# Kernel tuning notes

Hardware: AMD Instinct MI355X
Metric: run time of the kernel (lower is better)

## Reference

```python
import jax, jax.numpy as jnp
import numpy as np

B, D, H, W = 8, 768, 32, 32
C, K = 2, 8
COORD_DIM = 128
GRID = 16
DIST_THRESH = 5
NUM_STEPS = 3
STEP_SIZE = 0.1
HW = H * W


def _pair_indices():
    # Static grid of sampled points (stride = max(1, H//grid_size)) and all
    # ordered pairs with Manhattan distance in (0, 5] -- mirrors the torch loops.
    stride = max(1, H // GRID)
    pi, pj = np.meshgrid(np.arange(0, H, stride), np.arange(0, W, stride), indexing='ij')
    pi, pj = pi.ravel(), pj.ravel()
    d = np.abs(pi[:, None] - pi[None, :]) + np.abs(pj[:, None] - pj[None, :])
    a, b = np.nonzero((d > 0) & (d <= DIST_THRESH))
    return (pi[a] * W + pj[a]).astype(np.int32), (pi[b] * W + pj[b]).astype(np.int32)


def setup_inputs() -> dict:
    key = jax.random.key(0)
    ks = jax.random.split(key, 16)
    IN = 2 * D + COORD_DIM  # 1664

    def n(i, shape, s=1.0):
        return jax.random.normal(ks[i], shape, dtype=jnp.float32) * s

    return {
        'features': n(0, (B, D, H, W)),
        'cam_raw': jax.random.uniform(ks[1], (B, C, H, W), dtype=jnp.float32),
        'y_primary': jax.random.uniform(ks[2], (B, C), dtype=jnp.float32),
        'eps': n(3, (B, K)),
        'coord_emb': n(4, (256 * 256, COORD_DIM), 0.02),
        'aff_W1': n(5, (C, IN, 256), 0.02), 'aff_b1': jnp.zeros((C, 256), jnp.float32),
        'aff_W2': n(6, (C, 256, 128), 0.05), 'aff_b2': jnp.zeros((C, 128), jnp.float32),
        'aff_W3': n(7, (C, 128, 1), 0.05), 'aff_b3': jnp.zeros((C, 1), jnp.float32),
        'mu_W1': n(8, (D, 256), 0.02), 'mu_b1': jnp.zeros((256,), jnp.float32),
        'mu_W2': n(9, (256, K), 0.05), 'mu_b2': jnp.zeros((K,), jnp.float32),
        'ls_W1': n(10, (D, 256), 0.02), 'ls_b1': jnp.zeros((256,), jnp.float32),
        'ls_W2': n(11, (256, K), 0.05), 'ls_b2': jnp.zeros((K,), jnp.float32),
        'conf_scale': jnp.array(1.0, jnp.float32),
        'conf_bias': jnp.array(0.0, jnp.float32),
    }


def reference(features, cam_raw, y_primary, eps, coord_emb,
              aff_W1, aff_b1, aff_W2, aff_b2, aff_W3, aff_b3,
              mu_W1, mu_b1, mu_W2, mu_b2, ls_W1, ls_b1, ls_W2, ls_b2,
              conf_scale, conf_bias):
    idx_a_np, idx_b_np = _pair_indices()
    idx_a, idx_b = jnp.asarray(idx_a_np), jnp.asarray(idx_b_np)
    P = idx_a.shape[0]

    # --- SubClassPosterior on globally pooled features ---
    f_global = features.mean(axis=(2, 3))                      # (B, D)
    z_mu = jax.nn.relu(f_global @ mu_W1 + mu_b1) @ mu_W2 + mu_b2
    z_logstd = jax.nn.relu(f_global @ ls_W1 + ls_b1) @ ls_W2 + ls_b2
    z_samples = z_mu + jnp.exp(z_logstd) * eps

    # --- ClassConditionalAffinity: batched gather + grouped MLP over all pairs ---
    feat = features.reshape(B, D, HW)
    f1 = feat[:, :, idx_a].transpose(0, 2, 1)                  # (B, P, D)
    f2 = feat[:, :, idx_b].transpose(0, 2, 1)                  # (B, P, D)
    ce = 0.5 * (coord_emb[idx_a] + coord_emb[idx_b])           # (P, E)
    x = jnp.concatenate([f1, f2, jnp.broadcast_to(ce, (B, P, COORD_DIM))], axis=-1)
    h = jax.nn.relu(jnp.einsum('bpi,cio->bcpo', x, aff_W1) + aff_b1[:, None, :])
    h = jax.nn.relu(jnp.einsum('bcpi,cio->bcpo', h, aff_W2) + aff_b2[:, None, :])
    logit = (jnp.einsum('bcpi,cio->bcpo', h, aff_W3) + aff_b3[:, None, :])[..., 0]
    val = jax.nn.sigmoid(logit)                                # (B, C, P)

    # A = where(mask, sigmoid(mlp), I); pairs are strictly off-diagonal & unique
    A = jnp.broadcast_to(jnp.eye(HW, dtype=features.dtype), (B, C, HW, HW))
    A = A.at[:, :, idx_a, idx_b].set(val)
    A = A / (A.sum(axis=3, keepdims=True) + 1e-8)              # row-normalize

    # --- AnisotropicDiffusion: M <- M + dt * (A M - deg * M) ---
    M = cam_raw.reshape(B, C, HW)
    deg = A.sum(axis=3)                                        # (B, C, HW)
    for _ in range(NUM_STEPS):
        L = jnp.einsum('bcij,bcj->bci', A, M) - deg * M
        M = M + STEP_SIZE * L
    cam_refined = jnp.clip(M.reshape(B, C, H, W), 0.0, 1.0)

    confidence = jax.nn.sigmoid(conf_scale * cam_refined + conf_bias)
    return cam_refined, z_mu, z_logstd, z_samples, A, confidence
```

## Files before the change

### kernel.cpp

```cpp
#include <hip/hip_runtime.h>
#include <math.h>

#define BB 8
#define DD 768
#define HWN 1024
#define NS 256
#define PPAD 3072
#define O1 256
#define O2 128

typedef __attribute__((ext_vector_type(8))) short bf16x8;
typedef __attribute__((ext_vector_type(4))) float f32x4;

__constant__ int c_du[12] = {1,-1,0,0,2,-2,0,0,1, 1,-1,-1};
__constant__ int c_dv[12] = {0, 0,1,-1,0, 0,2,-2,1,-1, 1,-1};
__constant__ signed char c_rk[25] = {
  -1,-1, 5,-1,-1,
  -1,11, 1,10,-1,
   7, 3,-1, 2, 6,
  -1, 9, 0, 8,-1,
  -1,-1, 4,-1,-1};

__device__ inline ushort f2bf(float x) {
  unsigned u = __float_as_uint(x);
  u += 0x7FFF + ((u >> 16) & 1);
  return (ushort)(u >> 16);
}
__device__ inline float bf2f(ushort h) { return __uint_as_float(((unsigned)h) << 16); }

__device__ inline bool row_sampled(int row) {
  return ((row | (row >> 5)) & 1) == 0;
}

__global__ void __launch_bounds__(256) k1(const float* __restrict__ feat,
    const float* __restrict__ cemb, const float* __restrict__ W1,
    const float* __restrict__ b1, const float* __restrict__ W2,
    float* __restrict__ fg, ushort* __restrict__ g16,
    float* __restrict__ EH, ushort* __restrict__ WT16, ushort* __restrict__ W2T16,
    float* __restrict__ A) {
  __shared__ __align__(16) float sm[64 * 65];
  int blk = blockIdx.x;
  int t = threadIdx.x;
  if (blk < 6144) {
    int row = blk;
    const float4 v = reinterpret_cast<const float4*>(feat + (size_t)row * HWN)[t];
    float s = v.x + v.y + v.z + v.w;
#pragma unroll
    for (int m = 32; m >= 1; m >>= 1) s += __shfl_xor(s, m, 64);
    if ((t & 63) == 0) sm[t >> 6] = s;
    if ((t & 8) == 0) {
      int b = row / DD, d = row - b * DD;
      int u = t >> 4, r = t & 7;
      int s1 = u * 16 + 2 * r;
      g16[((size_t)(b * NS + s1)) * DD + d] = f2bf(v.x);
      g16[((size_t)(b * NS + s1 + 1)) * DD + d] = f2bf(v.z);
    }
    __syncthreads();
    if (t == 0) fg[row] = (sm[0] + sm[1] + sm[2] + sm[3]) * (1.0f / 1024.0f);
  } else if (blk < 6656) {
    int bs = blk - 6144;
    int c = bs >> 8, s = bs & 255;
    int u = s >> 4, v = s & 15;
    int pix = (u << 6) + (v << 1);
    float* ce = sm;
    if (t < 128) ce[t] = cemb[(size_t)pix * 128 + t];
    __syncthreads();
    const float* W = W1 + ((size_t)c * 1664 + 1536) * O1;
    float acc = 0.f;
    for (int e = 0; e < 128; e++) acc = fmaf(ce[e], W[(size_t)e * O1 + t], acc);
    EH[((size_t)(c * NS + s)) * O1 + t] = 0.5f * (acc + b1[c * O1 + t]);
  } else if (blk < 6864) {
    int r0 = blk - 6656;
    const float* src; ushort* dst; int K, N, k0, n0;
    if (r0 < 192) {
      int ch = r0 / 48, r = r0 % 48;
      int c = ch & 1, half = ch >> 1;
      src = W1 + ((size_t)c * 1664 + half * 768) * 256;
      dst = WT16 + (size_t)ch * 256 * 768;
      K = 768; N = 256; k0 = (r >> 2) * 64; n0 = (r & 3) * 64;
    } else {
      int r = r0 - 192;
      int c = r >> 3; int q = r & 7;
      src = W2 + (size_t)c * 256 * 128;
      dst = W2T16 + (size_t)c * 128 * 256;
      K = 256; N = 128; k0 = (q >> 1) * 64; n0 = (q & 1) * 64;
    }
    float (*T)[65] = reinterpret_cast<float(*)[65]>(sm);
    for (int i = 0; i < 16; i++) {
      int idx = i * 256 + t; int kl = idx >> 6, nl = idx & 63;
      T[kl][nl] = src[(size_t)(k0 + kl) * N + n0 + nl];
    }
    __syncthreads();
    for (int i = 0; i < 16; i++) {
      int idx = i * 256 + t; int nl = idx >> 6, kl = idx & 63;
      dst[(size_t)(n0 + nl) * K + k0 + kl] = f2bf(T[kl][nl]);
    }
  } else {
    int r0 = (blk - 6864) * 8;
#pragma unroll
    for (int i = 0; i < 8; i++) {
      int r_g = r0 + i;
      int row = r_g & 1023;
      if (!row_sampled(row)) {
        float4 o = make_float4(0.f, 0.f, 0.f, 0.f);
        if ((row >> 2) == t) {
          float dv = 1.0f / (1.0f + 1e-8f);
          int e = row & 3;
          if (e == 0) o.x = dv; else if (e == 1) o.y = dv;
          else if (e == 2) o.z = dv; else o.w = dv;
        }
        reinterpret_cast<float4*>(A + (size_t)r_g * 1024)[t] = o;
      }
    }
  }
}

__global__ void __launch_bounds__(256) k2(const ushort* __restrict__ g16,
    const ushort* __restrict__ WT16, const float* __restrict__ EHb,
    const float* __restrict__ fg, const float* __restrict__ muW1,
    const float* __restrict__ lsW1,
    ushort* __restrict__ Fb16, float* __restrict__ zscr) {
  __shared__ __align__(16) float sm[4096];
  int blk = blockIdx.x;
  int t = threadIdx.x;
  if (blk < 512) {
    int mt = blk & 31, nt = (blk >> 5) & 3, ch = blk >> 7;
    int c = ch & 1;
    int row0 = mt * 64, col0 = nt * 64;
    int wid = t >> 6, l = t & 63;
    int wm = wid & 1, wn = wid >> 1;
    int lm = l & 15, lk = (l >> 4) * 8;
    float (*ehs)[64] = reinterpret_cast<float(*)[64]>(sm);
    int s0 = row0 & 255;
    for (int i = 0; i < 16; i++) {
      int idx = i * 256 + t; int rl = idx >> 6, nl = idx & 63;
      ehs[rl][nl] = EHb[((size_t)(c * 256 + s0 + rl)) * 256 + col0 + nl];
    }
    f32x4 acc[2][2] = {};
    const ushort* ap0 = g16 + (size_t)(row0 + wm * 32 + lm) * DD + lk;
    const ushort* bp0 = WT16 + ((size_t)ch * 256 + col0 + wn * 32 + lm) * DD + lk;
#pragma unroll 4
    for (int k0 = 0; k0 < DD; k0 += 32) {
      bf16x8 a0 = *(const bf16x8*)(ap0 + k0);
      bf16x8 a1 = *(const bf16x8*)(ap0 + 16 * DD + k0);
      bf16x8 b0 = *(const bf16x8*)(bp0 + k0);
      bf16x8 b1 = *(const bf16x8*)(bp0 + 16 * DD + k0);
      acc[0][0] = __builtin_amdgcn_mfma_f32_16x16x32_bf16(a0, b0, acc[0][0], 0, 0, 0);
      acc[0][1] = __builtin_amdgcn_mfma_f32_16x16x32_bf16(a0, b1, acc[0][1], 0, 0, 0);
      acc[1][0] = __builtin_amdgcn_mfma_f32_16x16x32_bf16(a1, b0, acc[1][0], 0, 0, 0);
      acc[1][1] = __builtin_amdgcn_mfma_f32_16x16x32_bf16(a1, b1, acc[1][1], 0, 0, 0);
    }
    __syncthreads();
#pragma unroll
    for (int i = 0; i < 2; i++)
#pragma unroll
      for (int jj = 0; jj < 2; jj++)
#pragma unroll
        for (int r = 0; r < 4; r++) {
          int rm = wm * 32 + i * 16 + (l >> 4) * 4 + r;
          int cn = wn * 32 + jj * 16 + lm;
          float vo = acc[i][jj][r] + ehs[rm][cn];
          Fb16[((size_t)ch * 2048 + row0 + rm) * 256 + col0 + cn] = f2bf(vo);
        }
  } else {
    int i = blk - 512;
    int chunk = i % 6, path = (i / 6) & 1, b = i / 12;
    int rg = t >> 6, ct = t & 63;
    float* sf = sm;
    float (*red)[256] = reinterpret_cast<float(*)[256]>(sm + 128);
    if (t < 128) sf[t] = fg[b * DD + chunk * 128 + t];
    __syncthreads();
    const float* W = (path ? lsW1 : muW1) + (size_t)(chunk * 128) * 256;
    float acc[4] = {0.f, 0.f, 0.f, 0.f};
#pragma unroll 4
    for (int it = 0; it < 32; it++) {
      int d = it * 4 + rg;
      float f = sf[d];
      float4 w = *reinterpret_cast<const float4*>(W + (size_t)d * 256 + ct * 4);
      acc[0] = fmaf(f, w.x, acc[0]);
      acc[1] = fmaf(f, w.y, acc[1]);
      acc[2] = fmaf(f, w.z, acc[2]);
      acc[3] = fmaf(f, w.w, acc[3]);
    }
    *reinterpret_cast<float4*>(&red[rg][ct * 4]) =
        make_float4(acc[0], acc[1], acc[2], acc[3]);
    __syncthreads();
    zscr[(((size_t)(b * 2 + path)) * 6 + chunk) * 256 + t] =
        red[0][t] + red[1][t] + red[2][t] + red[3][t];
  }
}

__global__ void __launch_bounds__(256) k3(const ushort* __restrict__ Fb16,
    const ushort* __restrict__ W2T16, const float* __restrict__ b2,
    const float* __restrict__ W3, const float* __restrict__ b3,
    const float* __restrict__ zscr,
    const float* __restrict__ mub1, const float* __restrict__ muW2,
    const float* __restrict__ mub2,
    const float* __restrict__ lsb1, const float* __restrict__ lsW2,
    const float* __restrict__ lsb2, const float* __restrict__ eps,
    float* __restrict__ val,
    float* __restrict__ o_zmu, float* __restrict__ o_zls, float* __restrict__ o_zs,
    float* __restrict__ A) {
  __shared__ __align__(16) ushort h1s[64 * 256];
  __shared__ float psum2[2][64];
  __shared__ float sval[64];
  __shared__ float sinv[8];
  int blk = blockIdx.x;
  int t = threadIdx.x;
  if (blk < 832) {
    int bc = blk / 52, grp = blk - bc * 52;
    int b = bc >> 1, c = bc & 1;
    int site0 = grp * 5;
    int nsit = (site0 + 5 <= 256) ? 5 : (256 - site0);
    int npairs = nsit * 12;
    int wid = t >> 6, l = t & 63;
    int wm = wid & 1, wn = wid >> 1;
    int lm = l & 15, lk = (l >> 4) * 8;
    {
      int p_l = t >> 2, q = t & 3;
      int sl = p_l / 12, ko = p_l - sl * 12;
      bool realp = p_l < npairs;
      int s = site0 + (realp ? sl : 0);
      int u = s >> 4, v = s & 15;
      int ub = u + c_du[ko], vb = v + c_dv[ko];
      bool vld = realp && (ub >= 0) && (ub < 16) && (vb >= 0) && (vb < 16);
      int sb = vld ? ub * 16 + vb : s;
      const ushort* f1p = Fb16 + ((size_t)(c * 2048 + b * 256 + s)) * 256 + q * 64;
      const ushort* f2p = Fb16 + ((size_t)((2 + c) * 2048 + b * 256 + sb)) * 256 + q * 64;
      char* hb = (char*)h1s;
#pragma unroll
      for (int kk = 0; kk < 64; kk += 8) {
        bf16x8 x1 = *(const bf16x8*)(f1p + kk);
        bf16x8 x2 = *(const bf16x8*)(f2p + kk);
        bf16x8 o;
#pragma unroll
        for (int e = 0; e < 8; e++) {
          float a = bf2f((ushort)x1[e]) + bf2f((ushort)x2[e]);
          o[e] = (short)f2bf(fmaxf(a, 0.f));
        }
        int byt = (p_l * 512 + (q * 64 + kk) * 2) ^ ((p_l & 7) << 4);
        *(bf16x8*)(hb + byt) = o;
      }
    }
    __syncthreads();
    f32x4 acc[2][4] = {};
    const ushort* wp = W2T16 + ((size_t)(c * 128 + wn * 64 + lm)) * 256 + lk;
    const char* hb = (const char*)h1s;
    int p0 = wm * 32 + lm;
    int swz = (p0 & 7) << 4;
#pragma unroll 2
    for (int k0 = 0; k0 < 256; k0 += 32) {
      bf16x8 a0 = *(const bf16x8*)(hb + ((p0 * 512 + (k0 + lk) * 2) ^ swz));
      bf16x8 a1 = *(const bf16x8*)(hb + (((p0 + 16) * 512 + (k0 + lk) * 2) ^ swz));
#pragma unroll
      for (int nf = 0; nf < 4; nf++) {
        bf16x8 bb = *(const bf16x8*)(wp + nf * 16 * 256 + k0);
        acc[0][nf] = __builtin_amdgcn_mfma_f32_16x16x32_bf16(a0, bb, acc[0][nf], 0, 0, 0);
        acc[1][nf] = __builtin_amdgcn_mfma_f32_16x16x32_bf16(a1, bb, acc[1][nf], 0, 0, 0);
      }
    }
    float b2v[4], w3v[4];
#pragma unroll
    for (int nf = 0; nf < 4; nf++) {
      int col = wn * 64 + nf * 16 + lm;
      b2v[nf] = b2[c * 128 + col];
      w3v[nf] = W3[c * 128 + col];
    }
    float part[2][4];
#pragma unroll
    for (int mf = 0; mf < 2; mf++)
#pragma unroll
      for (int r = 0; r < 4; r++) {
        float ssum = 0.f;
#pragma unroll
        for (int nf = 0; nf < 4; nf++) {
          float h = fmaxf(acc[mf][nf][r] + b2v[nf], 0.f);
          ssum = fmaf(h, w3v[nf], ssum);
        }
        part[mf][r] = ssum;
      }
#pragma unroll
    for (int m = 1; m <= 8; m <<= 1)
#pragma unroll
      for (int mf = 0; mf < 2; mf++)
#pragma unroll
        for (int r = 0; r < 4; r++)
          part[mf][r] += __shfl_xor(part[mf][r], m, 64);
    if (lm == 0) {
#pragma unroll
      for (int mf = 0; mf < 2; mf++)
#pragma unroll
        for (int r = 0; r < 4; r++)
          psum2[wn][wm * 32 + mf * 16 + (l >> 4) * 4 + r] = part[mf][r];
    }
    __syncthreads();
    if (t < 64) {
      int pl = t;
      int sl2 = pl / 12, ko2 = pl - sl2 * 12;
      bool realp2 = pl < npairs;
      int ss = site0 + (realp2 ? sl2 : 0);
      int uu = ss >> 4, vv2 = ss & 15;
      int ub2 = uu + c_du[ko2], vb2 = vv2 + c_dv[ko2];
      bool vld2 = realp2 && (ub2 >= 0) && (ub2 < 16) && (vb2 >= 0) && (vb2 < 16);
      float lg = psum2[0][t] + psum2[1][t] + b3[c];
      float sv = 1.0f / (1.0f + expf(-lg));
      float outv = vld2 ? sv : 0.0f;
      sval[t] = outv;
      if (realp2) val[(size_t)bc * PPAD + site0 * 12 + pl] = outv;
    }
    __syncthreads();
    if (t < nsit) {
      float ssum = 1.f;
#pragma unroll
      for (int k = 0; k < 12; k++) ssum += sval[t * 12 + k];
      sinv[t] = 1.f / (ssum + 1e-8f);
    }
    __syncthreads();
    for (int sl3 = 0; sl3 < nsit; sl3++) {
      int ss = site0 + sl3;
      int uu = ss >> 4, vv = ss & 15;
      int row = uu * 64 + 2 * vv;
      size_t base = (size_t)bc * HWN * HWN + (size_t)row * HWN;
      float inv = sinv[sl3];
      float vo[4];
#pragma unroll
      for (int e = 0; e < 4; e++) {
        int col = t * 4 + e;
        float x = 0.f;
        if (col == row) {
          x = inv;
        } else if ((col & 33) == 0) {
          int cu = col >> 6, cv = (col & 31) >> 1;
          int du = cu - uu + 2, dv = cv - vv + 2;
          if (((unsigned)du < 5u) && ((unsigned)dv < 5u)) {
            int k = c_rk[du * 5 + dv];
            if (k >= 0) x = sval[sl3 * 12 + k] * inv;
          }
        }
        vo[e] = x;
      }
      reinterpret_cast<float4*>(A + base)[t] =
          make_float4(vo[0], vo[1], vo[2], vo[3]);
    }
  } else {
    int b = blk - 832;
    float* shm = (float*)h1s;
    float* shl = shm + 256;
    float* zres = shm + 512;
    float hm = mub1[t], hl = lsb1[t];
#pragma unroll
    for (int ch = 0; ch < 6; ch++) {
      hm += zscr[(((size_t)(b * 2 + 0)) * 6 + ch) * 256 + t];
      hl += zscr[(((size_t)(b * 2 + 1)) * 6 + ch) * 256 + t];
    }
    shm[t] = fmaxf(hm, 0.f);
    shl[t] = fmaxf(hl, 0.f);
    __syncthreads();
    if (t < 128 && (t & 63) < 8) {
      int path = t >> 6, kk = t & 7;
      const float* W2p = path ? lsW2 : muW2;
      const float* bi = path ? lsb2 : mub2;
      const float* sh = path ? shl : shm;
      float z = bi[kk];
      for (int i = 0; i < 256; i++) z = fmaf(sh[i], W2p[i * 8 + kk], z);
      zres[path * 8 + kk] = z;
    }
    __syncthreads();
    if (t < 8) {
      float zm = zres[t], zl = zres[8 + t];
      o_zmu[b * 8 + t] = zm;
      o_zls[b * 8 + t] = zl;
      o_zs[b * 8 + t] = zm + expf(zl) * eps[b * 8 + t];
    }
  }
}

__global__ void __launch_bounds__(256) k4(const float* __restrict__ cam,
    const float* __restrict__ val,
    const float* __restrict__ csc, const float* __restrict__ cbi,
    float* __restrict__ o_cam, float* __restrict__ o_conf) {
  __shared__ float M[NS];
  int bc = blockIdx.x;
  int t = threadIdx.x;
  int u = t >> 4, v = t & 15;
  int pix = (u << 6) + (v << 1);
  const float* camr = cam + (size_t)bc * HWN;
  float m = camr[pix];
  float vv[12];
  int nb[12];
  float ssum = 1.f;
#pragma unroll
  for (int k = 0; k < 12; k++) {
    int ub = u + c_du[k], vb = v + c_dv[k];
    bool vld = (ub >= 0) && (ub < 16) && (vb >= 0) && (vb < 16);
    nb[k] = vld ? ub * 16 + vb : t;
    vv[k] = vld ? val[(size_t)bc * PPAD + t * 12 + k] : 0.0f;
    ssum += vv[k];
  }
  float inv = 1.0f / (ssum + 1e-8f);
  float degn = ssum * inv;
  M[t] = m;
  __syncthreads();
  for (int step = 0; step < 3; step++) {
    float accv = m;
#pragma unroll
    for (int k = 0; k < 12; k++) accv = fmaf(vv[k], M[nb[k]], accv);
    float L = accv * inv - degn * m;
    m = fmaf(0.1f, L, m);
    __syncthreads();
    M[t] = m;
    __syncthreads();
  }
  float scale = csc[0], bias = cbi[0];
  for (int p = t; p < HWN; p += 256) {
    int ppi = p >> 5, ppj = p & 31;
    float x;
    if (((ppi | ppj) & 1) == 0) x = M[(ppi >> 1) * 16 + (ppj >> 1)];
    else x = camr[p];
    x = fminf(fmaxf(x, 0.0f), 1.0f);
    o_cam[(size_t)bc * HWN + p] = x;
    o_conf[(size_t)bc * HWN + p] = 1.0f / (1.0f + expf(-(scale * x + bias)));
  }
}

extern "C" void kernel_launch(void* const* d_in, const int* in_sizes, int n_in,
                              void* d_out, int out_size, void* d_ws, size_t ws_size,
                              hipStream_t stream) {
  const float* feat = (const float*)d_in[0];
  const float* cam  = (const float*)d_in[1];
  const float* eps  = (const float*)d_in[3];
  const float* cemb = (const float*)d_in[4];
  const float* aW1  = (const float*)d_in[5];
  const float* ab1  = (const float*)d_in[6];
  const float* aW2  = (const float*)d_in[7];
  const float* ab2  = (const float*)d_in[8];
  const float* aW3  = (const float*)d_in[9];
  const float* ab3  = (const float*)d_in[10];
  const float* muW1 = (const float*)d_in[11];
  const float* mub1 = (const float*)d_in[12];
  const float* muW2 = (const float*)d_in[13];
  const float* mub2 = (const float*)d_in[14];
  const float* lsW1 = (const float*)d_in[15];
  const float* lsb1 = (const float*)d_in[16];
  const float* lsW2 = (const float*)d_in[17];
  const float* lsb2 = (const float*)d_in[18];
  const float* csc  = (const float*)d_in[19];
  const float* cbi  = (const float*)d_in[20];

  float* out = (float*)d_out;
  float* o_cam  = out;
  float* o_zmu  = out + 16384;
  float* o_zls  = out + 16448;
  float* o_zs   = out + 16512;
  float* o_A    = out + 16576;
  float* o_conf = out + 16793792;

  float*  ws    = (float*)d_ws;
  float*  valb  = ws;
  float*  fg    = ws + 49152;
  float*  EHb   = ws + 55296;
  float*  zscr  = ws + 186368;
  ushort* g16   = (ushort*)(ws + 210944);
  ushort* WT16  = (ushort*)(ws + 997376);
  ushort* W2T16 = (ushort*)(ws + 1390592);
  ushort* Fb16  = (ushort*)(ws + 1423360);

  hipLaunchKernelGGL(k1, dim3(6864 + 2048), dim3(256), 0, stream,
                     feat, cemb, aW1, ab1, aW2, fg, g16, EHb, WT16, W2T16, o_A);
  hipLaunchKernelGGL(k2, dim3(608), dim3(256), 0, stream,
                     g16, WT16, EHb, fg, muW1, lsW1, Fb16, zscr);
  hipLaunchKernelGGL(k3, dim3(840), dim3(256), 0, stream,
                     Fb16, W2T16, ab2, aW3, ab3, zscr,
                     mub1, muW2, mub2, lsb1, lsW2, lsb2, eps,
                     valb, o_zmu, o_zls, o_zs, o_A);
  hipLaunchKernelGGL(k4, dim3(16), dim3(256), 0, stream,
                     cam, valb, csc, cbi, o_cam, o_conf);
}
```

Baseline: 84.15 us.

## Fuse diffusion kernel into k3 using per-(b,c) completion counters

Removes the separate k4 launch and moves the diffusion/confidence work into 16 extra blocks appended to k3. These blocks spin on atomic done counters, one per (b,c), until all 52 producer blocks for that slice have published their pair values. The counters are reset in k1. This saves one kernel launch and its tail gap, but it relies on the producer blocks being scheduled before or alongside the spinning consumers. It also adds atomic stores and fences on the val writes.

```diff
diff --git a/kernel.cpp b/kernel.cpp
--- a/kernel.cpp
+++ b/kernel.cpp
@@ -37,7 +37,7 @@
     const float* __restrict__ b1, const float* __restrict__ W2,
     float* __restrict__ fg, ushort* __restrict__ g16,
     float* __restrict__ EH, ushort* __restrict__ WT16, ushort* __restrict__ W2T16,
-    float* __restrict__ A) {
+    float* __restrict__ A, int* __restrict__ done) {
   __shared__ __align__(16) float sm[64 * 65];
   int blk = blockIdx.x;
   int t = threadIdx.x;
@@ -96,6 +96,9 @@
       dst[(size_t)(n0 + nl) * K + k0 + kl] = f2bf(T[kl][nl]);
     }
   } else {
+    if (blk == 6864 && t < 16) {
+      __hip_atomic_store(&done[t], 0, __ATOMIC_RELAXED, __HIP_MEMORY_SCOPE_AGENT);
+    }
     int r0 = (blk - 6864) * 8;
 #pragma unroll
     for (int i = 0; i < 8; i++) {
@@ -200,7 +203,10 @@
     const float* __restrict__ lsb2, const float* __restrict__ eps,
     float* __restrict__ val,
     float* __restrict__ o_zmu, float* __restrict__ o_zls, float* __restrict__ o_zs,
-    float* __restrict__ A) {
+    float* __restrict__ A, int* __restrict__ done,
+    const float* __restrict__ cam,
+    const float* __restrict__ csc, const float* __restrict__ cbi,
+    float* __restrict__ o_cam, float* __restrict__ o_conf) {
   __shared__ __align__(16) ushort h1s[64 * 256];
   __shared__ float psum2[2][64];
   __shared__ float sval[64];
@@ -306,7 +312,10 @@
       float sv = 1.0f / (1.0f + expf(-lg));
       float outv = vld2 ? sv : 0.0f;
       sval[t] = outv;
-      if (realp2) val[(size_t)bc * PPAD + site0 * 12 + pl] = outv;
+      if (realp2) {
+        __hip_atomic_store(&val[(size_t)bc * PPAD + site0 * 12 + pl], outv,
+                           __ATOMIC_RELAXED, __HIP_MEMORY_SCOPE_AGENT);
+      }
     }
     __syncthreads();
     if (t < nsit) {
@@ -342,7 +351,12 @@
       reinterpret_cast<float4*>(A + base)[t] =
           make_float4(vo[0], vo[1], vo[2], vo[3]);
     }
-  } else {
+    __syncthreads();
+    __threadfence();
+    if (t == 0) {
+      __hip_atomic_fetch_add(&done[bc], 1, __ATOMIC_RELEASE, __HIP_MEMORY_SCOPE_AGENT);
+    }
+  } else if (blk < 840) {
     int b = blk - 832;
     float* shm = (float*)h1s;
     float* shl = shm + 256;
@@ -372,54 +386,58 @@
       o_zls[b * 8 + t] = zl;
       o_zs[b * 8 + t] = zm + expf(zl) * eps[b * 8 + t];
     }
-  }
-}
-
-__global__ void __launch_bounds__(256) k4(const float* __restrict__ cam,
-    const float* __restrict__ val,
-    const float* __restrict__ csc, const float* __restrict__ cbi,
-    float* __restrict__ o_cam, float* __restrict__ o_conf) {
-  __shared__ float M[NS];
-  int bc = blockIdx.x;
-  int t = threadIdx.x;
-  int u = t >> 4, v = t & 15;
-  int pix = (u << 6) + (v << 1);
-  const float* camr = cam + (size_t)bc * HWN;
-  float m = camr[pix];
-  float vv[12];
-  int nb[12];
-  float ssum = 1.f;
-#pragma unroll
-  for (int k = 0; k < 12; k++) {
-    int ub = u + c_du[k], vb = v + c_dv[k];
-    bool vld = (ub >= 0) && (ub < 16) && (vb >= 0) && (vb < 16);
-    nb[k] = vld ? ub * 16 + vb : t;
-    vv[k] = vld ? val[(size_t)bc * PPAD + t * 12 + k] : 0.0f;
-    ssum += vv[k];
-  }
-  float inv = 1.0f / (ssum + 1e-8f);
-  float degn = ssum * inv;
-  M[t] = m;
-  __syncthreads();
-  for (int step = 0; step < 3; step++) {
-    float accv = m;
-#pragma unroll
-    for (int k = 0; k < 12; k++) accv = fmaf(vv[k], M[nb[k]], accv);
-    float L = accv * inv - degn * m;
-    m = fmaf(0.1f, L, m);
-    __syncthreads();
+  } else {
+    int bc = blk - 840;
+    float* M = (float*)h1s;
+    if (t == 0) {
+      while (__hip_atomic_load(&done[bc], __ATOMIC_ACQUIRE,
+                               __HIP_MEMORY_SCOPE_AGENT) != 52) {
+        __builtin_amdgcn_s_sleep(16);
+      }
+    }
+    __syncthreads();
+    __threadfence();
+    int u = t >> 4, v = t & 15;
+    int pix = (u << 6) + (v << 1);
+    const float* camr = cam + (size_t)bc * HWN;
+    float m = camr[pix];
+    float vv[12];
+    int nb[12];
+    float ssum = 1.f;
+#pragma unroll
+    for (int k = 0; k < 12; k++) {
+      int ub = u + c_du[k], vb = v + c_dv[k];
+      bool vld = (ub >= 0) && (ub < 16) && (vb >= 0) && (vb < 16);
+      nb[k] = vld ? ub * 16 + vb : t;
+      vv[k] = vld ? __hip_atomic_load(&val[(size_t)bc * PPAD + t * 12 + k],
+                                      __ATOMIC_RELAXED, __HIP_MEMORY_SCOPE_AGENT)
+                  : 0.0f;
+      ssum += vv[k];
+    }
+    float inv = 1.0f / (ssum + 1e-8f);
+    float degn = ssum * inv;
     M[t] = m;
     __syncthreads();
-  }
-  float scale = csc[0], bias = cbi[0];
-  for (int p = t; p < HWN; p += 256) {
-    int ppi = p >> 5, ppj = p & 31;
-    float x;
-    if (((ppi | ppj) & 1) == 0) x = M[(ppi >> 1) * 16 + (ppj >> 1)];
-    else x = camr[p];
-    x = fminf(fmaxf(x, 0.0f), 1.0f);
-    o_cam[(size_t)bc * HWN + p] = x;
-    o_conf[(size_t)bc * HWN + p] = 1.0f / (1.0f + expf(-(scale * x + bias)));
+    for (int step = 0; step < 3; step++) {
+      float accv = m;
+#pragma unroll
+      for (int k = 0; k < 12; k++) accv = fmaf(vv[k], M[nb[k]], accv);
+      float L = accv * inv - degn * m;
+      m = fmaf(0.1f, L, m);
+      __syncthreads();
+      M[t] = m;
+      __syncthreads();
+    }
+    float scale = csc[0], bias = cbi[0];
+    for (int p = t; p < HWN; p += 256) {
+      int ppi = p >> 5, ppj = p & 31;
+      float x;
+      if (((ppi | ppj) & 1) == 0) x = M[(ppi >> 1) * 16 + (ppj >> 1)];
+      else x = camr[p];
+      x = fminf(fmaxf(x, 0.0f), 1.0f);
+      o_cam[(size_t)bc * HWN + p] = x;
+      o_conf[(size_t)bc * HWN + p] = 1.0f / (1.0f + expf(-(scale * x + bias)));
+    }
   }
 }
 
@@ -464,15 +482,15 @@
   ushort* WT16  = (ushort*)(ws + 997376);
   ushort* W2T16 = (ushort*)(ws + 1390592);
   ushort* Fb16  = (ushort*)(ws + 1423360);
+  int*    done  = (int*)(ws + 2480000);
 
   hipLaunchKernelGGL(k1, dim3(6864 + 2048), dim3(256), 0, stream,
-                     feat, cemb, aW1, ab1, aW2, fg, g16, EHb, WT16, W2T16, o_A);
+                     feat, cemb, aW1, ab1, aW2, fg, g16, EHb, WT16, W2T16, o_A, done);
   hipLaunchKernelGGL(k2, dim3(608), dim3(256), 0, stream,
                      g16, WT16, EHb, fg, muW1, lsW1, Fb16, zscr);
-  hipLaunchKernelGGL(k3, dim3(840), dim3(256), 0, stream,
+  hipLaunchKernelGGL(k3, dim3(856), dim3(256), 0, stream,
                      Fb16, W2T16, ab2, aW3, ab3, zscr,
                      mub1, muW2, mub2, lsb1, lsW2, lsb2, eps,
-                     valb, o_zmu, o_zls, o_zs, o_A);
-  hipLaunchKernelGGL(k4, dim3(16), dim3(256), 0, stream,
-                     cam, valb, csc, cbi, o_cam, o_conf);
-}
+                     valb, o_zmu, o_zls, o_zs, o_A, done,
+                     cam, csc, cbi, o_cam, o_conf);
+}
```

Result: slower. 158.1 us (+87.9%).
